# Kernel optimization log

Hardware: AMD Instinct MI355X
Metric: run time of the kernel (lower is better)

Reference implementation:

```python
import jax, jax.numpy as jnp
import numpy as np

K = 7          # neighborhood kernel size (7x7)
NH = 8         # num heads


def _nbr_idx(n):
    # NATTEN-style clamped windows: window start = clip(i - K//2, 0, n-K)
    pos = jnp.arange(n)
    start = jnp.clip(pos - K // 2, 0, n - K)          # (n,)
    idx = start[:, None] + jnp.arange(K)[None, :]     # (n, K) absolute key positions
    rel = idx - pos[:, None] + (K - 1)                # (n, K) in [0, 2K-2] for rpb lookup
    return idx, rel


def _forward(x, w_qkv, b_qkv, rpb, w_proj, b_proj, w_fc1, b_fc1, w_fc2, b_fc2):
    B, C, H, W = x.shape
    hd = C // NH
    scale = hd ** -0.5

    # ---- neighborhood attention (norm0 = Identity) ----
    xp = jnp.transpose(x, (0, 2, 3, 1))                           # (B,H,W,C)
    qkv = xp @ w_qkv + b_qkv                                      # (B,H,W,3C)
    qkv = qkv.reshape(B, H, W, 3, NH, hd)
    q = qkv[:, :, :, 0] * scale                                   # (B,H,W,nh,hd)
    k = qkv[:, :, :, 1]
    v = qkv[:, :, :, 2]

    idx_h, rel_h = _nbr_idx(H)                                    # (H,K)
    idx_w, rel_w = _nbr_idx(W)                                    # (W,K)

    # gather 7x7 neighborhoods: (B,H,K,W,K,nh,hd)
    k_nbr = k[:, idx_h][:, :, :, idx_w]
    v_nbr = v[:, idx_h][:, :, :, idx_w]

    # attention logits: (B,H,W,nh,K,K)
    attn = jnp.einsum('bxynd,bxiyjnd->bxynij', q, k_nbr)
    # relative positional bias: rpb (nh, 2K-1, 2K-1) -> (nh,H,K,W,K)
    bias = rpb[:, rel_h][:, :, :, rel_w]                          # (nh,H,K,W,K)
    attn = attn + jnp.transpose(bias, (1, 3, 0, 2, 4))[None]      # (B,H,W,nh,K,K)

    attn = jax.nn.softmax(attn.reshape(B, H, W, NH, K * K), axis=-1)
    attn = attn.reshape(B, H, W, NH, K, K)

    out = jnp.einsum('bxynij,bxiyjnd->bxynd', attn, v_nbr)        # (B,H,W,nh,hd)
    out = out.reshape(B, H, W, C) @ w_proj + b_proj               # (B,H,W,C)
    x1 = jnp.transpose(out, (0, 3, 1, 2)) + x                     # residual skip0

    # ---- MLP (1x1-conv style, channels-first; norm1 = Identity) ----
    h = jnp.einsum('bchw,cf->bfhw', x1, w_fc1) + b_fc1[None, :, None, None]
    h = jax.nn.gelu(h, approximate=False)                         # torch nn.GELU (erf)
    y = jnp.einsum('bfhw,fc->bchw', h, w_fc2) + b_fc2[None, :, None, None]
    return y + x1                                                 # residual skip1


def setup_inputs() -> dict:
    key = jax.random.key(0)
    B, C, H, W = 1, 256, 64, 128
    hid = int(C * 2.0)
    ks = jax.random.split(key, 8)
    s = 0.02
    return {
        'x': jax.random.normal(ks[0], (B, C, H, W), jnp.float32),
        'w_qkv': jax.random.normal(ks[1], (C, 3 * C), jnp.float32) * s,
        'b_qkv': jnp.zeros((3 * C,), jnp.float32),
        'rpb': jax.random.normal(ks[2], (NH, 2 * K - 1, 2 * K - 1), jnp.float32) * s,
        'w_proj': jax.random.normal(ks[3], (C, C), jnp.float32) * s,
        'b_proj': jnp.zeros((C,), jnp.float32),
        'w_fc1': jax.random.normal(ks[4], (C, hid), jnp.float32) * s,
        'b_fc1': jnp.zeros((hid,), jnp.float32),
        'w_fc2': jax.random.normal(ks[5], (hid, C), jnp.float32) * s,
        'b_fc2': jnp.zeros((C,), jnp.float32),
    }


def reference(x, w_qkv, b_qkv, rpb, w_proj, b_proj, w_fc1, b_fc1, w_fc2, b_fc2):
    return _forward(x, w_qkv, b_qkv, rpb, w_proj, b_proj, w_fc1, b_fc1, w_fc2, b_fc2)
```

## Files before the change

### kernel.cpp

```cpp
#include <hip/hip_runtime.h>

typedef unsigned short ushort;
typedef short bf16x8 __attribute__((ext_vector_type(8)));
typedef float f32x4 __attribute__((ext_vector_type(4)));

static __device__ __forceinline__ ushort f2b(float f) {
  unsigned u = __builtin_bit_cast(unsigned, f);
  u = (u + 0x7fffu + ((u >> 16) & 1u)) >> 16;
  return (ushort)u;
}
static __device__ __forceinline__ float b2f(ushort b) {
  return __builtin_bit_cast(float, (unsigned)b << 16);
}

static __device__ __forceinline__ void gll16(const ushort* g, ushort* l) {
  __builtin_amdgcn_global_load_lds(
      (const __attribute__((address_space(1))) void*)g,
      (__attribute__((address_space(3))) void*)l, 16, 0, 0);
}

__global__ __launch_bounds__(256) void prep_kernel(
    const float* __restrict__ x,
    const float* __restrict__ w_qkv, const float* __restrict__ w_proj,
    const float* __restrict__ w_fc1, const float* __restrict__ w_fc2,
    ushort* __restrict__ xb, ushort* __restrict__ wqkvT,
    ushort* __restrict__ wprojT, ushort* __restrict__ wfc1T,
    ushort* __restrict__ wfc2T)
{
  __shared__ float tile[32][33];
  int t = blockIdx.x;
  const float* src; ushort* dst; int R, Nc, r0, c0;
  if (t < 2048)              { src = x;      dst = xb;     R = 256; Nc = 8192; r0 = (t >> 8) * 32; c0 = (t & 255) * 32; }
  else if ((t -= 2048) < 192){ src = w_qkv;  dst = wqkvT;  R = 256; Nc = 768;  r0 = (t / 24) * 32; c0 = (t % 24) * 32; }
  else if ((t -= 192) < 64)  { src = w_proj; dst = wprojT; R = 256; Nc = 256;  r0 = (t / 8) * 32;  c0 = (t % 8) * 32; }
  else if ((t -= 64) < 128)  { src = w_fc1;  dst = wfc1T;  R = 256; Nc = 512;  r0 = (t / 16) * 32; c0 = (t % 16) * 32; }
  else           { t -= 128;   src = w_fc2;  dst = wfc2T;  R = 512; Nc = 256;  r0 = (t / 8) * 32;  c0 = (t % 8) * 32; }

  const int tx = threadIdx.x & 31, ty = threadIdx.x >> 5;
  #pragma unroll
  for (int i = 0; i < 4; i++)
    tile[ty + i * 8][tx] = src[(size_t)(r0 + ty + i * 8) * Nc + c0 + tx];
  __syncthreads();
  #pragma unroll
  for (int i = 0; i < 4; i++)
    dst[(size_t)(c0 + ty + i * 8) * R + r0 + tx] = f2b(tile[tx][ty + i * 8]);
}

template<int EPI, int KD>
__global__ __launch_bounds__(256) void gemm_mfma(
    const ushort* __restrict__ A, const ushort* __restrict__ Bt,
    const float* __restrict__ bias, const float* __restrict__ R,
    const ushort* __restrict__ RS,
    void* __restrict__ C0, void* __restrict__ C1,
    int M, int N)
{
  __shared__ __attribute__((aligned(16))) ushort As[64 * 128];
  __shared__ __attribute__((aligned(16))) ushort Bs[64 * 128];

  const int bm = blockIdx.y * 64;
  const int bn = blockIdx.x * 64;
  const int t  = threadIdx.x;
  const int w    = t >> 6;
  const int lane = t & 63;
  const int wm = (w & 1) * 32;
  const int wn = (w >> 1) * 32;
  const int lm = lane & 15;
  const int kq = lane >> 4;

  const int rl  = lane >> 4;
  const int cbx = (lane & 15) << 4;
  const int xr  = (lm & 7) << 4;

  f32x4 acc[2][2] = {};

  #pragma unroll
  for (int k0 = 0; k0 < KD; k0 += 128) {
    #pragma unroll
    for (int s = 0; s < 4; s++) {
      const int c = w * 4 + s;
      const int r = c * 4 + rl;
      const int off = (cbx ^ ((r & 7) << 4)) >> 1;
      gll16(A  + (size_t)(bm + r) * KD + k0 + off, As + c * 512);
      gll16(Bt + (size_t)(bn + r) * KD + k0 + off, Bs + c * 512);
    }
    __syncthreads();

    #pragma unroll
    for (int ks = 0; ks < 4; ks++) {
      const int kb = ks * 64 + (kq << 4);
      const int cs = kb ^ xr;
      bf16x8 a0 = *(const bf16x8*)((const char*)As + (wm + lm)      * 256 + cs);
      bf16x8 a1 = *(const bf16x8*)((const char*)As + (wm + 16 + lm) * 256 + cs);
      bf16x8 b0 = *(const bf16x8*)((const char*)Bs + (wn + lm)      * 256 + cs);
      bf16x8 b1 = *(const bf16x8*)((const char*)Bs + (wn + 16 + lm) * 256 + cs);
      acc[0][0] = __builtin_amdgcn_mfma_f32_16x16x32_bf16(a0, b0, acc[0][0], 0, 0, 0);
      acc[0][1] = __builtin_amdgcn_mfma_f32_16x16x32_bf16(a0, b1, acc[0][1], 0, 0, 0);
      acc[1][0] = __builtin_amdgcn_mfma_f32_16x16x32_bf16(a1, b0, acc[1][0], 0, 0, 0);
      acc[1][1] = __builtin_amdgcn_mfma_f32_16x16x32_bf16(a1, b1, acc[1][1], 0, 0, 0);
    }
    __syncthreads();
  }

  #pragma unroll
  for (int ti = 0; ti < 2; ti++) {
    #pragma unroll
    for (int tj = 0; tj < 2; tj++) {
      const int n  = bn + wn + tj * 16 + lm;
      const int m0 = bm + wm + ti * 16 + kq * 4;
      if (EPI == 0) {
        if (n < 512) {
          #pragma unroll
          for (int r = 0; r < 4; r++)
            ((ushort*)C0)[(size_t)(m0 + r) * N + n] = f2b(acc[ti][tj][r] + bias[n]);
        } else {
          ushort4 st;
          st.x = f2b(acc[ti][tj][0] + bias[n]);
          st.y = f2b(acc[ti][tj][1] + bias[n]);
          st.z = f2b(acc[ti][tj][2] + bias[n]);
          st.w = f2b(acc[ti][tj][3] + bias[n]);
          *(ushort4*)((ushort*)C1 + (size_t)(n - 512) * 8192 + m0) = st;
        }
      }
    }
  }
}

__global__ __launch_bounds__(256, 4) void natt_mfma(
    const ushort* __restrict__ qkv, const ushort* __restrict__ vT,
    const float* __restrict__ rpb, ushort* __restrict__ att)
{
  __shared__ __attribute__((aligned(16))) ushort Plds[4][7][16][40];
  __shared__ float Rlds[4][176];

  const int w    = threadIdx.x >> 6;
  const int lane = threadIdx.x & 63;
  const int l  = lane & 15;
  const int q  = lane >> 4;
  const int tile = blockIdx.x;
  const int n    = blockIdx.y * 4 + w;
  const int ph  = tile >> 3;
  const int pw0 = (tile & 7) << 4;
  const int p0  = ph * 128 + pw0;

  int sh = ph - 3;  sh = sh < 0 ? 0 : (sh > 57 ? 57 : sh);
  int sb = pw0 - 3; sb = sb < 0 ? 0 : sb;
  const int sba = sb & ~7;

  const float L2E = 1.44269504f;
  for (int idx = lane; idx < 169; idx += 64)
    Rlds[w][idx] = rpb[n * 169 + idx] * L2E;

  bf16x8 qf = *(const bf16x8*)(qkv + (size_t)(p0 + l) * 768 + n * 32 + q * 8);

  const float KSC = 0.17677669529663689f * 1.44269504f;
  const int relh0 = sh - ph + 6;
  float rsum[4] = {0.f, 0.f, 0.f, 0.f};

  #pragma unroll
  for (int h = 0; h < 2; h++) {
    f32x4 s[7] = {};
    #pragma unroll
    for (int i = 0; i < 7; i++) {
      const int rowp = (sh + i) * 128;
      int jc = sba + h * 16 + l;
      jc = jc > 127 ? 127 : jc;
      bf16x8 kf = *(const bf16x8*)(qkv + (size_t)(rowp + jc) * 768 + 256 + n * 32 + q * 8);
      s[i] = __builtin_amdgcn_mfma_f32_16x16x32_bf16(qf, kf, s[i], 0, 0, 0);
    }
    #pragma unroll
    for (int r = 0; r < 4; r++) {
      const int pw = pw0 + q * 4 + r;
      int sw = pw - 3; sw = sw < 0 ? 0 : (sw > 121 ? 121 : sw);
      const int jc = sba + h * 16 + l;
      const bool valid = (unsigned)(jc - sw) <= 6u;
      int relw = jc - pw + 6;
      relw = relw < 0 ? 0 : (relw > 12 ? 12 : relw);
      #pragma unroll
      for (int i = 0; i < 7; i++) {
        float b = Rlds[w][(relh0 + i) * 13 + relw];
        float v = s[i][r] * KSC + b;
        v = valid ? v : -1e30f;
        float e = exp2f(v);
        rsum[r] += e;
        Plds[w][i][q * 4 + r][h * 16 + l] = f2b(e);
      }
    }
  }

  #pragma unroll
  for (int r = 0; r < 4; r++) {
    rsum[r] += __shfl_xor(rsum[r], 1);
    rsum[r] += __shfl_xor(rsum[r], 2);
    rsum[r] += __shfl_xor(rsum[r], 4);
    rsum[r] += __shfl_xor(rsum[r], 8);
  }

  f32x4 o[2] = {};
  #pragma unroll
  for (int i = 0; i < 7; i++) {
    bf16x8 pf = *(const bf16x8*)(&Plds[w][i][l][q * 8]);
    const int rowp = (sh + i) * 128;
    #pragma unroll
    for (int dh = 0; dh < 2; dh++) {
      bf16x8 vf = *(const bf16x8*)(vT + (size_t)(n * 32 + dh * 16 + l) * 8192
                                      + rowp + sba + q * 8);
      o[dh] = __builtin_amdgcn_mfma_f32_16x16x32_bf16(pf, vf, o[dh], 0, 0, 0);
    }
  }

  #pragma unroll
  for (int r = 0; r < 4; r++) {
    const float inv = 1.0f / rsum[r];
    #pragma unroll
    for (int dh = 0; dh < 2; dh++)
      att[(size_t)(p0 + q * 4 + r) * 256 + n * 32 + dh * 16 + l] = f2b(o[dh][r] * inv);
  }
}

__global__ __launch_bounds__(512) void mlp_fused(
    const ushort* __restrict__ att, const ushort* __restrict__ wprojT,
    const ushort* __restrict__ wfc1T, const ushort* __restrict__ wfc2T,
    const float* __restrict__ b_proj, const float* __restrict__ b_fc1,
    const float* __restrict__ b_fc2, const float* __restrict__ xres,
    float* __restrict__ out)
{
  __shared__ __attribute__((aligned(16))) ushort Bs[128 * 128];
  __shared__ __attribute__((aligned(16))) ushort X1[32 * 256];
  __shared__ __attribute__((aligned(16))) ushort Hs[32 * 256];

  const int bm   = blockIdx.x * 32;
  const int t    = threadIdx.x;
  const int w    = t >> 6;
  const int lane = t & 63;
  const int lm   = lane & 15;
  const int kq   = lane >> 4;
  const int wm   = (w & 1) * 16;
  const int wnn  = (w >> 1) * 32;

  const int rl  = lane >> 4;
  const int swl = (lane & 15) << 3;

  auto stageB = [&](const ushort* __restrict__ src, int ldk, int row0, int col0) {
    #pragma unroll
    for (int s = 0; s < 4; s++) {
      const int c = w * 4 + s;
      const int n = c * 4 + rl;
      gll16(src + (size_t)(row0 + n) * ldk + col0 + (swl ^ ((n & 7) << 3)),
            Bs + c * 512);
    }
  };

  f32x4 acc_o[4] = {};

  #pragma unroll
  for (int nh = 0; nh < 2; nh++) {
    f32x4 accp[2] = {};
    #pragma unroll
    for (int kt = 0; kt < 2; kt++) {
      stageB(wprojT, 256, nh * 128, kt * 128);
      __syncthreads();
      #pragma unroll
      for (int ks = 0; ks < 4; ks++) {
        const int kc = ks * 32 + kq * 8;
        bf16x8 a = *(const bf16x8*)(att + (size_t)(bm + wm + lm) * 256 + kt * 128 + kc);
        #pragma unroll
        for (int tj = 0; tj < 2; tj++) {
          const int n = wnn + tj * 16 + lm;
          bf16x8 b = *(const bf16x8*)(&Bs[n * 128 + (kc ^ ((n & 7) << 3))]);
          accp[tj] = __builtin_amdgcn_mfma_f32_16x16x32_bf16(a, b, accp[tj], 0, 0, 0);
        }
      }
      __syncthreads();
    }
    #pragma unroll
    for (int tj = 0; tj < 2; tj++) {
      const int n  = nh * 128 + wnn + tj * 16 + lm;
      const int m0 = wm + kq * 4;
      const float bp = b_proj[n];
      float4 xr = *(const float4*)(xres + (size_t)n * 8192 + bm + m0);
      const float* xp = &xr.x;
      #pragma unroll
      for (int r = 0; r < 4; r++) {
        const int m = m0 + r;
        X1[m * 256 + (n ^ ((m & 7) << 3))] = f2b(accp[tj][r] + bp + xp[r]);
      }
    }
  }
  __syncthreads();

  #pragma unroll
  for (int hf = 0; hf < 2; hf++) {
    #pragma unroll
    for (int nh = 0; nh < 2; nh++) {
      f32x4 acch[2] = {};
      #pragma unroll
      for (int kt = 0; kt < 2; kt++) {
        stageB(wfc1T, 256, hf * 256 + nh * 128, kt * 128);
        __syncthreads();
        #pragma unroll
        for (int ks = 0; ks < 4; ks++) {
          const int kc = ks * 32 + kq * 8;
          const int ar = wm + lm;
          const int ac = kt * 128 + kc;
          bf16x8 a = *(const bf16x8*)(&X1[ar * 256 + (ac ^ ((ar & 7) << 3))]);
          #pragma unroll
          for (int tj = 0; tj < 2; tj++) {
            const int n = wnn + tj * 16 + lm;
            bf16x8 b = *(const bf16x8*)(&Bs[n * 128 + (kc ^ ((n & 7) << 3))]);
            acch[tj] = __builtin_amdgcn_mfma_f32_16x16x32_bf16(a, b, acch[tj], 0, 0, 0);
          }
        }
        __syncthreads();
      }
      #pragma unroll
      for (int tj = 0; tj < 2; tj++) {
        const int n  = nh * 128 + wnn + tj * 16 + lm;
        const float bf = b_fc1[hf * 256 + n];
        #pragma unroll
        for (int r = 0; r < 4; r++) {
          const int m = wm + kq * 4 + r;
          float v = acch[tj][r] + bf;
          v = 0.5f * v * (1.0f + erff(v * 0.70710678118f));
          Hs[m * 256 + (n ^ ((m & 7) << 3))] = f2b(v);
        }
      }
    }
    __syncthreads();

    #pragma unroll
    for (int nh = 0; nh < 2; nh++) {
      #pragma unroll
      for (int kt = 0; kt < 2; kt++) {
        stageB(wfc2T, 512, nh * 128, hf * 256 + kt * 128);
        __syncthreads();
        #pragma unroll
        for (int ks = 0; ks < 4; ks++) {
          const int kc = ks * 32 + kq * 8;
          const int ar = wm + lm;
          const int ac = kt * 128 + kc;
          bf16x8 a = *(const bf16x8*)(&Hs[ar * 256 + (ac ^ ((ar & 7) << 3))]);
          #pragma unroll
          for (int tj = 0; tj < 2; tj++) {
            const int n = wnn + tj * 16 + lm;
            bf16x8 b = *(const bf16x8*)(&Bs[n * 128 + (kc ^ ((n & 7) << 3))]);
            acc_o[nh * 2 + tj] =
                __builtin_amdgcn_mfma_f32_16x16x32_bf16(a, b, acc_o[nh * 2 + tj], 0, 0, 0);
          }
        }
        __syncthreads();
      }
    }
  }

  #pragma unroll
  for (int nh = 0; nh < 2; nh++) {
    #pragma unroll
    for (int tj = 0; tj < 2; tj++) {
      const int n  = nh * 128 + wnn + tj * 16 + lm;
      const int m0 = wm + kq * 4;
      const float bf = b_fc2[n];
      float4 v;
      float* vp = &v.x;
      #pragma unroll
      for (int r = 0; r < 4; r++) {
        const int m = m0 + r;
        vp[r] = acc_o[nh * 2 + tj][r] + bf + b2f(X1[m * 256 + (n ^ ((m & 7) << 3))]);
      }
      *(float4*)(out + (size_t)n * 8192 + bm + m0) = v;
    }
  }
}

extern "C" void kernel_launch(void* const* d_in, const int* in_sizes, int n_in,
                              void* d_out, int out_size, void* d_ws, size_t ws_size,
                              hipStream_t stream)
{
  const float* x      = (const float*)d_in[0];
  const float* w_qkv  = (const float*)d_in[1];
  const float* b_qkv  = (const float*)d_in[2];
  const float* rpb    = (const float*)d_in[3];
  const float* w_proj = (const float*)d_in[4];
  const float* b_proj = (const float*)d_in[5];
  const float* w_fc1  = (const float*)d_in[6];
  const float* b_fc1  = (const float*)d_in[7];
  const float* w_fc2  = (const float*)d_in[8];
  const float* b_fc2  = (const float*)d_in[9];
  float* out = (float*)d_out;

  const int M = 8192;
  char* ws = (char*)d_ws;
  ushort* xb     = (ushort*)(ws);
  ushort* qkv    = (ushort*)(ws + 4194304);
  ushort* wqkvT  = (ushort*)(ws + 20971520);
  ushort* wprojT = (ushort*)(ws + 21364736);
  ushort* wfc1T  = (ushort*)(ws + 21495808);
  ushort* wfc2T  = (ushort*)(ws + 21757952);
  ushort* vT     = (ushort*)(ws + 22020096);
  ushort* att = xb;

  dim3 blk(256);

  prep_kernel<<<dim3(2560), blk, 0, stream>>>(
      x, w_qkv, w_proj, w_fc1, w_fc2, xb, wqkvT, wprojT, wfc1T, wfc2T);

  gemm_mfma<0, 256><<<dim3(768 / 64, M / 64), blk, 0, stream>>>(
      xb, wqkvT, b_qkv, nullptr, nullptr, qkv, vT, M, 768);

  natt_mfma<<<dim3(512, 2), blk, 0, stream>>>(qkv, vT, rpb, att);

  mlp_fused<<<dim3(256), dim3(512), 0, stream>>>(
      att, wprojT, wfc1T, wfc2T, b_proj, b_fc1, b_fc2, x, out);
}
```

Measured before the change: 138.6 us.

## Double-buffer weight tiles in fused MLP kernel and hoist operand loads

```diff
diff --git a/kernel.cpp b/kernel.cpp
--- a/kernel.cpp
+++ b/kernel.cpp
@@ -224,7 +224,7 @@
     const float* __restrict__ b_fc2, const float* __restrict__ xres,
     float* __restrict__ out)
 {
-  __shared__ __attribute__((aligned(16))) ushort Bs[128 * 128];
+  __shared__ __attribute__((aligned(16))) ushort Bs[2][128 * 128];
   __shared__ __attribute__((aligned(16))) ushort X1[32 * 256];
   __shared__ __attribute__((aligned(16))) ushort Hs[32 * 256];
 
@@ -236,139 +236,162 @@
   const int kq   = lane >> 4;
   const int wm   = (w & 1) * 16;
   const int wnn  = (w >> 1) * 32;
-
-  const int rl  = lane >> 4;
-  const int swl = (lane & 15) << 3;
-
-  auto stageB = [&](const ushort* __restrict__ src, int ldk, int row0, int col0) {
+  const int rl   = lane >> 4;
+  const int swl  = (lane & 15) << 3;
+
+  bf16x8 af[2][4];
+  #pragma unroll
+  for (int kt = 0; kt < 2; kt++)
+    #pragma unroll
+    for (int ks = 0; ks < 4; ks++)
+      af[kt][ks] = *(const bf16x8*)(att + (size_t)(bm + wm + lm) * 256
+                                    + kt * 128 + ks * 32 + kq * 8);
+  float4 xr4[2][2];
+  float bpv[2][2], bf1v[2][2][2], bf2v[2][2];
+  #pragma unroll
+  for (int nh = 0; nh < 2; nh++)
+    #pragma unroll
+    for (int tj = 0; tj < 2; tj++) {
+      const int n = nh * 128 + wnn + tj * 16 + lm;
+      xr4[nh][tj]     = *(const float4*)(xres + (size_t)n * 8192 + bm + wm + kq * 4);
+      bpv[nh][tj]     = b_proj[n];
+      bf1v[0][nh][tj] = b_fc1[n];
+      bf1v[1][nh][tj] = b_fc1[256 + n];
+      bf2v[nh][tj]    = b_fc2[n];
+    }
+
+  auto stage = [&](int b, const ushort* __restrict__ src, int ldk, int row0, int col0) {
     #pragma unroll
     for (int s = 0; s < 4; s++) {
       const int c = w * 4 + s;
       const int n = c * 4 + rl;
       gll16(src + (size_t)(row0 + n) * ldk + col0 + (swl ^ ((n & 7) << 3)),
-            Bs + c * 512);
+            &Bs[b][c * 512]);
     }
   };
-
-  f32x4 acc_o[4] = {};
-
-  #pragma unroll
-  for (int nh = 0; nh < 2; nh++) {
-    f32x4 accp[2] = {};
-    #pragma unroll
-    for (int kt = 0; kt < 2; kt++) {
-      stageB(wprojT, 256, nh * 128, kt * 128);
-      __syncthreads();
-      #pragma unroll
-      for (int ks = 0; ks < 4; ks++) {
-        const int kc = ks * 32 + kq * 8;
-        bf16x8 a = *(const bf16x8*)(att + (size_t)(bm + wm + lm) * 256 + kt * 128 + kc);
-        #pragma unroll
-        for (int tj = 0; tj < 2; tj++) {
-          const int n = wnn + tj * 16 + lm;
-          bf16x8 b = *(const bf16x8*)(&Bs[n * 128 + (kc ^ ((n & 7) << 3))]);
-          accp[tj] = __builtin_amdgcn_mfma_f32_16x16x32_bf16(a, b, accp[tj], 0, 0, 0);
-        }
-      }
-      __syncthreads();
-    }
+  auto compP = [&](int b, int kt, f32x4* a2) {
+    #pragma unroll
+    for (int ks = 0; ks < 4; ks++) {
+      const int kc = ks * 32 + kq * 8;
+      #pragma unroll
+      for (int tj = 0; tj < 2; tj++) {
+        const int n = wnn + tj * 16 + lm;
+        bf16x8 bfr = *(const bf16x8*)(&Bs[b][n * 128 + (kc ^ ((n & 7) << 3))]);
+        a2[tj] = __builtin_amdgcn_mfma_f32_16x16x32_bf16(af[kt][ks], bfr, a2[tj], 0, 0, 0);
+      }
+    }
+  };
+  auto compS = [&](int b, const ushort* __restrict__ S, int kt, f32x4* a2) {
+    #pragma unroll
+    for (int ks = 0; ks < 4; ks++) {
+      const int kc = ks * 32 + kq * 8;
+      const int ar = wm + lm;
+      const int ac = kt * 128 + kc;
+      bf16x8 a = *(const bf16x8*)(S + ar * 256 + (ac ^ ((ar & 7) << 3)));
+      #pragma unroll
+      for (int tj = 0; tj < 2; tj++) {
+        const int n = wnn + tj * 16 + lm;
+        bf16x8 bfr = *(const bf16x8*)(&Bs[b][n * 128 + (kc ^ ((n & 7) << 3))]);
+        a2[tj] = __builtin_amdgcn_mfma_f32_16x16x32_bf16(a, bfr, a2[tj], 0, 0, 0);
+      }
+    }
+  };
+  auto projEpi = [&](int nh, f32x4* a2) {
+    #pragma unroll
+    for (int tj = 0; tj < 2; tj++) {
+      const int n = nh * 128 + wnn + tj * 16 + lm;
+      const float* xp = (const float*)&xr4[nh][tj];
+      #pragma unroll
+      for (int r = 0; r < 4; r++) {
+        const int m = wm + kq * 4 + r;
+        X1[m * 256 + (n ^ ((m & 7) << 3))] = f2b(a2[tj][r] + bpv[nh][tj] + xp[r]);
+      }
+    }
+  };
+  auto fc1Epi = [&](int hf, int nh, f32x4* a2) {
+    #pragma unroll
+    for (int tj = 0; tj < 2; tj++) {
+      const int n = nh * 128 + wnn + tj * 16 + lm;
+      #pragma unroll
+      for (int r = 0; r < 4; r++) {
+        const int m = wm + kq * 4 + r;
+        float v = a2[tj][r] + bf1v[hf][nh][tj];
+        v = 0.5f * v * (1.0f + erff(v * 0.70710678118f));
+        Hs[m * 256 + (n ^ ((m & 7) << 3))] = f2b(v);
+      }
+    }
+  };
+
+  f32x4 accp[2][2] = {};
+  f32x4 acch[2]    = {};
+  f32x4 acco[2][2] = {};
+
+  stage(0, wprojT, 256, 0, 0);
+
+  __syncthreads(); stage(1, wprojT, 256,   0, 128);
+  compP(0, 0, accp[0]);
+  __syncthreads(); stage(0, wprojT, 256, 128,   0);
+  compP(1, 1, accp[0]); projEpi(0, accp[0]);
+  __syncthreads(); stage(1, wprojT, 256, 128, 128);
+  compP(0, 0, accp[1]);
+  __syncthreads(); stage(0, wfc1T, 256,   0,   0);
+  compP(1, 1, accp[1]); projEpi(1, accp[1]);
+
+  __syncthreads(); stage(1, wfc1T, 256,   0, 128);
+  compS(0, X1, 0, acch);
+  __syncthreads(); stage(0, wfc1T, 256, 128,   0);
+  compS(1, X1, 1, acch); fc1Epi(0, 0, acch);
+  acch[0] = f32x4{}; acch[1] = f32x4{};
+  __syncthreads(); stage(1, wfc1T, 256, 128, 128);
+  compS(0, X1, 0, acch);
+  __syncthreads(); stage(0, wfc2T, 512,   0,   0);
+  compS(1, X1, 1, acch); fc1Epi(0, 1, acch);
+  acch[0] = f32x4{}; acch[1] = f32x4{};
+
+  __syncthreads(); stage(1, wfc2T, 512,   0, 128);
+  compS(0, Hs, 0, acco[0]);
+  __syncthreads(); stage(0, wfc2T, 512, 128,   0);
+  compS(1, Hs, 1, acco[0]);
+  __syncthreads(); stage(1, wfc2T, 512, 128, 128);
+  compS(0, Hs, 0, acco[1]);
+  __syncthreads(); stage(0, wfc1T, 256, 256,   0);
+  compS(1, Hs, 1, acco[1]);
+
+  __syncthreads(); stage(1, wfc1T, 256, 256, 128);
+  compS(0, X1, 0, acch);
+  __syncthreads(); stage(0, wfc1T, 256, 384,   0);
+  compS(1, X1, 1, acch); fc1Epi(1, 0, acch);
+  acch[0] = f32x4{}; acch[1] = f32x4{};
+  __syncthreads(); stage(1, wfc1T, 256, 384, 128);
+  compS(0, X1, 0, acch);
+  __syncthreads(); stage(0, wfc2T, 512,   0, 256);
+  compS(1, X1, 1, acch); fc1Epi(1, 1, acch);
+
+  __syncthreads(); stage(1, wfc2T, 512,   0, 384);
+  compS(0, Hs, 0, acco[0]);
+  __syncthreads(); stage(0, wfc2T, 512, 128, 256);
+  compS(1, Hs, 1, acco[0]);
+  __syncthreads(); stage(1, wfc2T, 512, 128, 384);
+  compS(0, Hs, 0, acco[1]);
+  __syncthreads();
+  compS(1, Hs, 1, acco[1]);
+
+  #pragma unroll
+  for (int nh = 0; nh < 2; nh++)
     #pragma unroll
     for (int tj = 0; tj < 2; tj++) {
       const int n  = nh * 128 + wnn + tj * 16 + lm;
       const int m0 = wm + kq * 4;
-      const float bp = b_proj[n];
-      float4 xr = *(const float4*)(xres + (size_t)n * 8192 + bm + m0);
-      const float* xp = &xr.x;
+      float4 v;
+      float* vp = &v.x;
       #pragma unroll
       for (int r = 0; r < 4; r++) {
         const int m = m0 + r;
-        X1[m * 256 + (n ^ ((m & 7) << 3))] = f2b(accp[tj][r] + bp + xp[r]);
-      }
-    }
-  }
-  __syncthreads();
-
-  #pragma unroll
-  for (int hf = 0; hf < 2; hf++) {
-    #pragma unroll
-    for (int nh = 0; nh < 2; nh++) {
-      f32x4 acch[2] = {};
-      #pragma unroll
-      for (int kt = 0; kt < 2; kt++) {
-        stageB(wfc1T, 256, hf * 256 + nh * 128, kt * 128);
-        __syncthreads();
-        #pragma unroll
-        for (int ks = 0; ks < 4; ks++) {
-          const int kc = ks * 32 + kq * 8;
-          const int ar = wm + lm;
-          const int ac = kt * 128 + kc;
-          bf16x8 a = *(const bf16x8*)(&X1[ar * 256 + (ac ^ ((ar & 7) << 3))]);
-          #pragma unroll
-          for (int tj = 0; tj < 2; tj++) {
-            const int n = wnn + tj * 16 + lm;
-            bf16x8 b = *(const bf16x8*)(&Bs[n * 128 + (kc ^ ((n & 7) << 3))]);
-            acch[tj] = __builtin_amdgcn_mfma_f32_16x16x32_bf16(a, b, acch[tj], 0, 0, 0);
-          }
-        }
-        __syncthreads();
-      }
-      #pragma unroll
-      for (int tj = 0; tj < 2; tj++) {
-        const int n  = nh * 128 + wnn + tj * 16 + lm;
-        const float bf = b_fc1[hf * 256 + n];
-        #pragma unroll
-        for (int r = 0; r < 4; r++) {
-          const int m = wm + kq * 4 + r;
-          float v = acch[tj][r] + bf;
-          v = 0.5f * v * (1.0f + erff(v * 0.70710678118f));
-          Hs[m * 256 + (n ^ ((m & 7) << 3))] = f2b(v);
-        }
-      }
-    }
-    __syncthreads();
-
-    #pragma unroll
-    for (int nh = 0; nh < 2; nh++) {
-      #pragma unroll
-      for (int kt = 0; kt < 2; kt++) {
-        stageB(wfc2T, 512, nh * 128, hf * 256 + kt * 128);
-        __syncthreads();
-        #pragma unroll
-        for (int ks = 0; ks < 4; ks++) {
-          const int kc = ks * 32 + kq * 8;
-          const int ar = wm + lm;
-          const int ac = kt * 128 + kc;
-          bf16x8 a = *(const bf16x8*)(&Hs[ar * 256 + (ac ^ ((ar & 7) << 3))]);
-          #pragma unroll
-          for (int tj = 0; tj < 2; tj++) {
-            const int n = wnn + tj * 16 + lm;
-            bf16x8 b = *(const bf16x8*)(&Bs[n * 128 + (kc ^ ((n & 7) << 3))]);
-            acc_o[nh * 2 + tj] =
-                __builtin_amdgcn_mfma_f32_16x16x32_bf16(a, b, acc_o[nh * 2 + tj], 0, 0, 0);
-          }
-        }
-        __syncthreads();
-      }
-    }
-  }
-
-  #pragma unroll
-  for (int nh = 0; nh < 2; nh++) {
-    #pragma unroll
-    for (int tj = 0; tj < 2; tj++) {
-      const int n  = nh * 128 + wnn + tj * 16 + lm;
-      const int m0 = wm + kq * 4;
-      const float bf = b_fc2[n];
-      float4 v;
-      float* vp = &v.x;
-      #pragma unroll
-      for (int r = 0; r < 4; r++) {
-        const int m = m0 + r;
-        vp[r] = acc_o[nh * 2 + tj][r] + bf + b2f(X1[m * 256 + (n ^ ((m & 7) << 3))]);
+        vp[r] = acco[nh][tj][r] + bf2v[nh][tj]
+              + b2f(X1[m * 256 + (n ^ ((m & 7) << 3))]);
       }
       *(float4*)(out + (size_t)n * 8192 + bm + m0) = v;
     }
-  }
 }
 
 extern "C" void kernel_launch(void* const* d_in, const int* in_sizes, int n_in,
```

Measured after the change: 133.9 us. 3.3% less time.
